# Kernel tuning notes

Hardware: AMD Instinct MI355X
Metric: run time of the kernel (lower is better)

The kernel has to match this reference:

```python
import jax, jax.numpy as jnp
import numpy as np

B, N, D = 4, 2048, 256
H = 8
HD = D // H
FF = 1024
EPS = 1e-5


def layer_norm(x, g, b):
    mu = jnp.mean(x, axis=-1, keepdims=True)
    var = jnp.mean((x - mu) ** 2, axis=-1, keepdims=True)
    return (x - mu) * jax.lax.rsqrt(var + EPS) * g + b


def setup_inputs() -> dict:
    key = jax.random.key(0)
    ks = jax.random.split(key, 12)
    s = 0.02
    return {
        "tokens": jax.random.normal(ks[0], (B, N, D), dtype=jnp.float32),
        "key_padding_mask": jnp.zeros((B, N), dtype=bool),
        "ln1_g": jnp.ones((D,), jnp.float32),
        "ln1_b": jnp.zeros((D,), jnp.float32),
        "wq": jax.random.normal(ks[1], (D, D), jnp.float32) * s,
        "bq": jnp.zeros((D,), jnp.float32),
        "wk": jax.random.normal(ks[2], (D, D), jnp.float32) * s,
        "bk": jnp.zeros((D,), jnp.float32),
        "wv": jax.random.normal(ks[3], (D, D), jnp.float32) * s,
        "bv": jnp.zeros((D,), jnp.float32),
        "wo": jax.random.normal(ks[4], (D, D), jnp.float32) * s,
        "bo": jnp.zeros((D,), jnp.float32),
        "ln2_g": jnp.ones((D,), jnp.float32),
        "ln2_b": jnp.zeros((D,), jnp.float32),
        "w1": jax.random.normal(ks[5], (D, FF), jnp.float32) * s,
        "b1": jnp.zeros((FF,), jnp.float32),
        "w2": jax.random.normal(ks[6], (FF, D), jnp.float32) * s,
        "b2": jnp.zeros((D,), jnp.float32),
    }


def reference(tokens, key_padding_mask, ln1_g, ln1_b, wq, bq, wk, bk, wv, bv,
              wo, bo, ln2_g, ln2_b, w1, b1, w2, b2):
    x = tokens
    # --- self-attention sublayer (pre-LN) ---
    xn = layer_norm(x, ln1_g, ln1_b)
    q = (xn @ wq + bq).reshape(B, N, H, HD).transpose(0, 2, 1, 3)  # [B,H,N,HD]
    k = (xn @ wk + bk).reshape(B, N, H, HD).transpose(0, 2, 1, 3)
    v = (xn @ wv + bv).reshape(B, N, H, HD).transpose(0, 2, 1, 3)
    scores = jnp.einsum('bhqd,bhkd->bhqk', q, k) / np.sqrt(HD).astype(np.float32)
    scores = jnp.where(key_padding_mask[:, None, None, :], -jnp.inf, scores)
    probs = jax.nn.softmax(scores, axis=-1)
    attn = jnp.einsum('bhqk,bhkd->bhqd', probs, v)
    attn = attn.transpose(0, 2, 1, 3).reshape(B, N, D)
    x = x + (attn @ wo + bo)
    # --- feed-forward sublayer (pre-LN) ---
    xn2 = layer_norm(x, ln2_g, ln2_b)
    h = jax.nn.gelu(xn2 @ w1 + b1, approximate=False)  # torch GELU is exact erf
    x = x + (h @ w2 + b2)
    return x
```

## Files before the change

### kernel.cpp

```cpp
#include <hip/hip_runtime.h>
#include <cmath>

typedef __attribute__((ext_vector_type(8))) __bf16 bf16x8;
typedef __attribute__((ext_vector_type(4))) __bf16 bf16x4;
typedef __attribute__((ext_vector_type(4))) float  f32x4;

constexpr int NB   = 4;
constexpr int SEQ  = 2048;
constexpr int DM   = 256;
constexpr int NH   = 8;
constexpr int DH   = 32;
constexpr int DFF  = 1024;
constexpr int MTOK = NB * SEQ;

__global__ __launch_bounds__(256) void ln_kernel(const float* __restrict__ x,
                                                 const float* __restrict__ g,
                                                 const float* __restrict__ b,
                                                 __bf16* __restrict__ out) {
  int wave = threadIdx.x >> 6, lane = threadIdx.x & 63;
  int row = blockIdx.x * 4 + wave;
  const float* xr = x + (size_t)row * DM;
  f32x4 v = *(const f32x4*)(xr + lane * 4);
  float s  = v[0] + v[1] + v[2] + v[3];
  float sq = v[0]*v[0] + v[1]*v[1] + v[2]*v[2] + v[3]*v[3];
  #pragma unroll
  for (int off = 1; off < 64; off <<= 1) {
    s  += __shfl_xor(s, off);
    sq += __shfl_xor(sq, off);
  }
  float mu  = s * (1.0f / DM);
  float var = sq * (1.0f / DM) - mu * mu;
  float rs  = rsqrtf(var + 1e-5f);
  f32x4 gv = *(const f32x4*)(g + lane * 4);
  f32x4 bv = *(const f32x4*)(b + lane * 4);
  bf16x4 o;
  #pragma unroll
  for (int i = 0; i < 4; ++i) o[i] = (__bf16)((v[i] - mu) * rs * gv[i] + bv[i]);
  *(bf16x4*)(out + (size_t)row * DM + lane * 4) = o;
}

__global__ __launch_bounds__(256) void prep_kernel(
    const float* __restrict__ wq, const float* __restrict__ wk, const float* __restrict__ wv,
    const float* __restrict__ wo, const float* __restrict__ w1, const float* __restrict__ w2,
    const unsigned char* __restrict__ mask, const float* __restrict__ tokens,
    const float* __restrict__ ln1g, const float* __restrict__ ln1b,
    __bf16* __restrict__ wqkvT, __bf16* __restrict__ woT,
    __bf16* __restrict__ w1T, __bf16* __restrict__ w2T,
    float* __restrict__ madd_g, __bf16* __restrict__ xn1) {
  __shared__ float tile[32][33];
  int z = blockIdx.z;
  int tid = threadIdx.x;
  if (z == 6) {
    if (blockIdx.x) return;
    int idx = blockIdx.y * 256 + tid;
    madd_g[idx] = mask[idx] ? -__builtin_inff() : 0.0f;
    return;
  }
  if (z >= 7) {
    int lb = blockIdx.y * 32 + blockIdx.x;
    int row = (z - 7) * 4096 + lb * 4 + (tid >> 6);
    int lane = tid & 63;
    const float* xr = tokens + (size_t)row * DM;
    f32x4 v = *(const f32x4*)(xr + lane * 4);
    float s  = v[0] + v[1] + v[2] + v[3];
    float sq = v[0]*v[0] + v[1]*v[1] + v[2]*v[2] + v[3]*v[3];
    #pragma unroll
    for (int off = 1; off < 64; off <<= 1) {
      s  += __shfl_xor(s, off);
      sq += __shfl_xor(sq, off);
    }
    float mu  = s * (1.0f / DM);
    float var = sq * (1.0f / DM) - mu * mu;
    float rs  = rsqrtf(var + 1e-5f);
    f32x4 gv = *(const f32x4*)(ln1g + lane * 4);
    f32x4 bv = *(const f32x4*)(ln1b + lane * 4);
    bf16x4 o;
    #pragma unroll
    for (int i = 0; i < 4; ++i) o[i] = (__bf16)((v[i] - mu) * rs * gv[i] + bv[i]);
    *(bf16x4*)(xn1 + (size_t)row * DM + lane * 4) = o;
    return;
  }
  const float* W; __bf16* Wt; int K, N;
  if      (z == 0) { W = wq; Wt = wqkvT;          K = 256;  N = 256;  }
  else if (z == 1) { W = wk; Wt = wqkvT + 65536;  K = 256;  N = 256;  }
  else if (z == 2) { W = wv; Wt = wqkvT + 131072; K = 256;  N = 256;  }
  else if (z == 3) { W = wo; Wt = woT;            K = 256;  N = 256;  }
  else if (z == 4) { W = w1; Wt = w1T;            K = 256;  N = 1024; }
  else             { W = w2; Wt = w2T;            K = 1024; N = 256;  }
  int n0 = blockIdx.x * 32, k0 = blockIdx.y * 32;
  if (n0 >= N || k0 >= K) return;
  {
    int kl = tid >> 3, n4 = (tid & 7) * 4;
    f32x4 v = *(const f32x4*)(W + (size_t)(k0 + kl) * N + n0 + n4);
    tile[kl][n4 + 0] = v[0]; tile[kl][n4 + 1] = v[1];
    tile[kl][n4 + 2] = v[2]; tile[kl][n4 + 3] = v[3];
  }
  __syncthreads();
  {
    int nl = tid >> 3, k4 = (tid & 7) * 4;
    bf16x4 o;
    #pragma unroll
    for (int i = 0; i < 4; ++i) o[i] = (__bf16)tile[k4 + i][nl];
    *(bf16x4*)(Wt + (size_t)(n0 + nl) * K + k0 + k4) = o;
  }
}

__global__ __launch_bounds__(256) void transpose_v(const __bf16* __restrict__ V,
                                                   __bf16* __restrict__ Vt) {
  __shared__ __bf16 tile[64][40];
  int tok0 = blockIdx.x * 64;
  int bh = blockIdx.y;
  int tid = threadIdx.x;
  {
    int tl = tid >> 2, h8 = (tid & 3) * 8;
    *(bf16x8*)&tile[tl][h8] = *(const bf16x8*)(V + ((size_t)bh * SEQ + tok0 + tl) * DH + h8);
  }
  __syncthreads();
  {
    int hl = tid >> 3, t8 = (tid & 7) * 8;
    bf16x8 o;
    #pragma unroll
    for (int i = 0; i < 8; ++i) o[i] = tile[t8 + i][hl];
    *(bf16x8*)(Vt + ((size_t)bh * DH + hl) * SEQ + tok0 + t8) = o;
  }
}

template<int BM, int BN, int EP>
__global__ __launch_bounds__(256) void gemm_bt(
    const __bf16* __restrict__ A, const __bf16* __restrict__ Bt,
    int M, int N, int K,
    const float* __restrict__ bias,
    const float* __restrict__ bq, const float* __restrict__ bk, const float* __restrict__ bv,
    const float* __restrict__ resid, float* __restrict__ outf,
    __bf16* __restrict__ outb,
    __bf16* __restrict__ outq, __bf16* __restrict__ outk, __bf16* __restrict__ outv) {
  constexpr int MT = BM / 32, NT = BN / 32;
  __shared__ __bf16 As[BM][72];
  __shared__ __bf16 Bs[BN][72];
  int tid = threadIdx.x;
  int wave = tid >> 6, lane = tid & 63;
  int wm = wave >> 1, wn = wave & 1;
  int quad = lane >> 4, l16 = lane & 15;
  int m0 = blockIdx.x * BM, n0 = blockIdx.y * BN;

  f32x4 acc[MT][NT];
  #pragma unroll
  for (int mt = 0; mt < MT; ++mt)
    #pragma unroll
    for (int nt = 0; nt < NT; ++nt)
      #pragma unroll
      for (int r = 0; r < 4; ++r) acc[mt][nt][r] = 0.0f;

  for (int kt = 0; kt < K; kt += 64) {
    __syncthreads();
    #pragma unroll
    for (int p = 0; p < BM / 32; ++p) {
      int idx = p * 256 + tid, row = idx >> 3, c8 = (idx & 7) * 8;
      *(bf16x8*)&As[row][c8] = *(const bf16x8*)(A + (size_t)(m0 + row) * K + kt + c8);
    }
    #pragma unroll
    for (int p = 0; p < BN / 32; ++p) {
      int idx = p * 256 + tid, row = idx >> 3, c8 = (idx & 7) * 8;
      *(bf16x8*)&Bs[row][c8] = *(const bf16x8*)(Bt + (size_t)(n0 + row) * K + kt + c8);
    }
    __syncthreads();
    #pragma unroll
    for (int ks = 0; ks < 2; ++ks) {
      bf16x8 af[MT], bfr[NT];
      #pragma unroll
      for (int mt = 0; mt < MT; ++mt)
        af[mt] = *(const bf16x8*)&As[wm * (BM / 2) + mt * 16 + l16][ks * 32 + quad * 8];
      #pragma unroll
      for (int nt = 0; nt < NT; ++nt)
        bfr[nt] = *(const bf16x8*)&Bs[wn * (BN / 2) + nt * 16 + l16][ks * 32 + quad * 8];
      #pragma unroll
      for (int mt = 0; mt < MT; ++mt)
        #pragma unroll
        for (int nt = 0; nt < NT; ++nt)
          acc[mt][nt] = __builtin_amdgcn_mfma_f32_16x16x32_bf16(af[mt], bfr[nt], acc[mt][nt], 0, 0, 0);
    }
  }

  #pragma unroll
  for (int mt = 0; mt < MT; ++mt)
  #pragma unroll
  for (int nt = 0; nt < NT; ++nt)
  #pragma unroll
  for (int r = 0; r < 4; ++r) {
    int gm = m0 + wm * (BM / 2) + mt * 16 + quad * 4 + r;
    int gn = n0 + wn * (BN / 2) + nt * 16 + l16;
    float v = acc[mt][nt][r];
    if constexpr (EP == 0) {
      int which = gn >> 8, nn = gn & 255;
      const float* bp = which == 0 ? bq : (which == 1 ? bk : bv);
      v += bp[nn];
      int h = nn >> 5, hd = nn & 31;
      int bb = gm >> 11, tok = gm & 2047;
      __bf16* dst = which == 0 ? outq : (which == 1 ? outk : outv);
      dst[(((size_t)(bb * NH + h)) * SEQ + tok) * DH + hd] = (__bf16)v;
    } else if constexpr (EP == 1) {
      v += bias[gn] + resid[(size_t)gm * N + gn];
      outf[(size_t)gm * N + gn] = v;
    } else {
      v += bias[gn];
      outb[(size_t)gm * N + gn] = (__bf16)(0.5f * v * (1.0f + erff(v * 0.70710678118654752f)));
    }
  }
}

__global__ __launch_bounds__(256) void attn_kernel(
    const __bf16* __restrict__ Q, const __bf16* __restrict__ K,
    const __bf16* __restrict__ Vt, const float* __restrict__ madd_g,
    __bf16* __restrict__ out) {
  constexpr float C2 = 0.2550350030061664f;
  __shared__ __bf16 Ks[64][40];
  __shared__ __bf16 Vs[48][72];
  __shared__ __bf16 Ps[4][16][72];
  int bh = blockIdx.x;
  int q0 = blockIdx.y * 64;
  int b  = bh >> 3, h = bh & 7;
  int tid = threadIdx.x;
  int wave = tid >> 6, lane = tid & 63;
  int quad = lane >> 4, l16 = lane & 15;
  const __bf16* Qb = Q  + (size_t)bh * SEQ * DH;
  const __bf16* Kb = K  + (size_t)bh * SEQ * DH;
  const __bf16* Vb = Vt + (size_t)bh * DH * SEQ;
  const float* maddb = madd_g + b * SEQ;
  int qw = q0 + wave * 16;

  if (tid < 32) ((unsigned int*)&Vs[32][0])[tid] = 0x3F803F80u;

  bf16x8 qf = *(const bf16x8*)(Qb + (size_t)(qw + l16) * DH + quad * 8);

  f32x4 o[2], ol;
  #pragma unroll
  for (int nt = 0; nt < 2; ++nt)
    #pragma unroll
    for (int r = 0; r < 4; ++r) o[nt][r] = 0.0f;
  #pragma unroll
  for (int r = 0; r < 4; ++r) ol[r] = 0.0f;

  for (int kt = 0; kt < SEQ / 64; ++kt) {
    int k0 = kt * 64;
    __syncthreads();
    { int row = tid >> 2, c8 = (tid & 3) * 8;
      *(bf16x8*)&Ks[row][c8] = *(const bf16x8*)(Kb + (size_t)(k0 + row) * DH + c8); }
    { int row = tid >> 3, c8 = (tid & 7) * 8;
      *(bf16x8*)&Vs[row][c8] = *(const bf16x8*)(Vb + (size_t)row * SEQ + k0 + c8); }
    __syncthreads();

    f32x4 md[4];
    #pragma unroll
    for (int mt = 0; mt < 4; ++mt)
      md[mt] = *(const f32x4*)(maddb + k0 + mt * 16 + quad * 4);

    f32x4 s[4];
    f32x4 zf; zf[0] = zf[1] = zf[2] = zf[3] = 0.0f;
    #pragma unroll
    for (int mt = 0; mt < 4; ++mt) {
      bf16x8 kf = *(const bf16x8*)&Ks[mt * 16 + l16][quad * 8];
      s[mt] = __builtin_amdgcn_mfma_f32_16x16x32_bf16(kf, qf, zf, 0, 0, 0);
    }

    #pragma unroll
    for (int mt = 0; mt < 4; ++mt) {
      bf16x4 pv;
      #pragma unroll
      for (int r = 0; r < 4; ++r)
        pv[r] = (__bf16)exp2f(fmaf(s[mt][r], C2, md[mt][r]));
      *(bf16x4*)&Ps[wave][l16][mt * 16 + quad * 4] = pv;
    }

    #pragma unroll
    for (int ks = 0; ks < 2; ++ks) {
      bf16x8 pf = *(const bf16x8*)&Ps[wave][l16][ks * 32 + quad * 8];
      #pragma unroll
      for (int nt = 0; nt < 2; ++nt) {
        bf16x8 vf = *(const bf16x8*)&Vs[nt * 16 + l16][ks * 32 + quad * 8];
        o[nt] = __builtin_amdgcn_mfma_f32_16x16x32_bf16(pf, vf, o[nt], 0, 0, 0);
      }
      bf16x8 vf1 = *(const bf16x8*)&Vs[32 + l16][ks * 32 + quad * 8];
      ol = __builtin_amdgcn_mfma_f32_16x16x32_bf16(pf, vf1, ol, 0, 0, 0);
    }
  }

  float inv[4];
  #pragma unroll
  for (int r = 0; r < 4; ++r) inv[r] = 1.0f / __shfl(ol[r], quad * 16);
  #pragma unroll
  for (int nt = 0; nt < 2; ++nt)
  #pragma unroll
  for (int r = 0; r < 4; ++r) {
    int q   = qw + quad * 4 + r;
    int col = h * DH + nt * 16 + l16;
    out[((size_t)(b * SEQ + q)) * DM + col] = (__bf16)(o[nt][r] * inv[r]);
  }
}

extern "C" void kernel_launch(void* const* d_in, const int* in_sizes, int n_in,
                              void* d_out, int out_size, void* d_ws, size_t ws_size,
                              hipStream_t stream) {
  const float* tokens = (const float*)d_in[0];
  const unsigned char* mask = (const unsigned char*)d_in[1];
  const float* ln1g = (const float*)d_in[2];
  const float* ln1b = (const float*)d_in[3];
  const float* wq = (const float*)d_in[4];
  const float* bq = (const float*)d_in[5];
  const float* wk = (const float*)d_in[6];
  const float* bk = (const float*)d_in[7];
  const float* wv = (const float*)d_in[8];
  const float* bv = (const float*)d_in[9];
  const float* wo = (const float*)d_in[10];
  const float* bo = (const float*)d_in[11];
  const float* ln2g = (const float*)d_in[12];
  const float* ln2b = (const float*)d_in[13];
  const float* w1 = (const float*)d_in[14];
  const float* b1 = (const float*)d_in[15];
  const float* w2 = (const float*)d_in[16];
  const float* b2 = (const float*)d_in[17];
  float* out = (float*)d_out;
  char* ws = (char*)d_ws;

  __bf16* wqkvT = (__bf16*)(ws + 0);
  __bf16* woT   = (__bf16*)(ws + 393216);
  __bf16* w1T   = (__bf16*)(ws + 524288);
  __bf16* w2T   = (__bf16*)(ws + 1048576);
  __bf16* xn1   = (__bf16*)(ws + 1572864);
  __bf16* qb    = (__bf16*)(ws + 5767168);
  __bf16* kb    = (__bf16*)(ws + 9961472);
  __bf16* vb    = (__bf16*)(ws + 14155776);
  __bf16* vt    = (__bf16*)(ws + 18350080);
  __bf16* attn  = (__bf16*)(ws + 22544384);
  float*  x1    = (float*)(ws + 26738688);
  __bf16* xn2   = (__bf16*)(ws + 35127296);
  __bf16* hbuf  = (__bf16*)(ws + 39321600);
  float*  madd  = (float*)(ws + 56098816);

  prep_kernel<<<dim3(32, 32, 9), 256, 0, stream>>>(
      wq, wk, wv, wo, w1, w2, mask, tokens, ln1g, ln1b,
      wqkvT, woT, w1T, w2T, madd, xn1);

  gemm_bt<64, 64, 0><<<dim3(128, 12), 256, 0, stream>>>(
      xn1, wqkvT, MTOK, 768, 256, nullptr, bq, bk, bv,
      nullptr, nullptr, nullptr, qb, kb, vb);

  transpose_v<<<dim3(SEQ / 64, 32), 256, 0, stream>>>(vb, vt);

  attn_kernel<<<dim3(32, SEQ / 64), 256, 0, stream>>>(qb, kb, vt, madd, attn);

  gemm_bt<64, 64, 1><<<dim3(128, 4), 256, 0, stream>>>(
      attn, woT, MTOK, 256, 256, bo, nullptr, nullptr, nullptr,
      tokens, x1, nullptr, nullptr, nullptr, nullptr);

  ln_kernel<<<MTOK / 4, 256, 0, stream>>>(x1, ln2g, ln2b, xn2);

  gemm_bt<64, 64, 2><<<dim3(128, 16), 256, 0, stream>>>(
      xn2, w1T, MTOK, DFF, 256, b1, nullptr, nullptr, nullptr,
      nullptr, nullptr, hbuf, nullptr, nullptr, nullptr);

  gemm_bt<64, 64, 1><<<dim3(128, 4), 256, 0, stream>>>(
      hbuf, w2T, MTOK, 256, DFF, b2, nullptr, nullptr, nullptr,
      x1, out, nullptr, nullptr, nullptr, nullptr);
}
```

Baseline: 215.3 us.

## Enlarge attention key tile, use register ones for rowsum, retile GEMMs

The attention kernel now processes 128 keys per iteration instead of 64, which halves the number of block barriers and tile loads. The row-sum MFMA takes a register vector of ones instead of an extra row of ones in shared memory, which also removes the final shuffle. exp2f becomes the hardware builtin, and the mask load moves into the exp loop. All GEMM launches switch to larger 128-row (and 128-column) tiles, giving fewer blocks, higher reuse and more LDS per block, at the risk of lower occupancy and poorer wave balance across CUs.

```diff
diff --git a/kernel.cpp b/kernel.cpp
--- a/kernel.cpp
+++ b/kernel.cpp
@@ -213,9 +213,9 @@
     const __bf16* __restrict__ Vt, const float* __restrict__ madd_g,
     __bf16* __restrict__ out) {
   constexpr float C2 = 0.2550350030061664f;
-  __shared__ __bf16 Ks[64][40];
-  __shared__ __bf16 Vs[48][72];
-  __shared__ __bf16 Ps[4][16][72];
+  __shared__ __bf16 Ks[128][40];
+  __shared__ __bf16 Vs[32][136];
+  __shared__ __bf16 Ps[4][16][136];
   int bh = blockIdx.x;
   int q0 = blockIdx.y * 64;
   int b  = bh >> 3, h = bh & 7;
@@ -228,10 +228,12 @@
   const float* maddb = madd_g + b * SEQ;
   int qw = q0 + wave * 16;
 
-  if (tid < 32) ((unsigned int*)&Vs[32][0])[tid] = 0x3F803F80u;
-
   bf16x8 qf = *(const bf16x8*)(Qb + (size_t)(qw + l16) * DH + quad * 8);
 
+  bf16x8 ones;
+  #pragma unroll
+  for (int i = 0; i < 8; ++i) ones[i] = (__bf16)1.0f;
+
   f32x4 o[2], ol;
   #pragma unroll
   for (int nt = 0; nt < 2; ++nt)
@@ -240,60 +242,60 @@
   #pragma unroll
   for (int r = 0; r < 4; ++r) ol[r] = 0.0f;
 
-  for (int kt = 0; kt < SEQ / 64; ++kt) {
-    int k0 = kt * 64;
+  for (int kt = 0; kt < SEQ / 128; ++kt) {
+    int k0 = kt * 128;
     __syncthreads();
-    { int row = tid >> 2, c8 = (tid & 3) * 8;
-      *(bf16x8*)&Ks[row][c8] = *(const bf16x8*)(Kb + (size_t)(k0 + row) * DH + c8); }
-    { int row = tid >> 3, c8 = (tid & 7) * 8;
-      *(bf16x8*)&Vs[row][c8] = *(const bf16x8*)(Vb + (size_t)row * SEQ + k0 + c8); }
+    #pragma unroll
+    for (int p = 0; p < 2; ++p) {
+      int idx = p * 256 + tid, row = idx >> 2, c8 = (idx & 3) * 8;
+      *(bf16x8*)&Ks[row][c8] = *(const bf16x8*)(Kb + (size_t)(k0 + row) * DH + c8);
+    }
+    #pragma unroll
+    for (int p = 0; p < 2; ++p) {
+      int idx = p * 256 + tid, row = idx >> 4, c8 = (idx & 15) * 8;
+      *(bf16x8*)&Vs[row][c8] = *(const bf16x8*)(Vb + (size_t)row * SEQ + k0 + c8);
+    }
     __syncthreads();
 
-    f32x4 md[4];
-    #pragma unroll
-    for (int mt = 0; mt < 4; ++mt)
-      md[mt] = *(const f32x4*)(maddb + k0 + mt * 16 + quad * 4);
-
-    f32x4 s[4];
+    f32x4 s[8];
     f32x4 zf; zf[0] = zf[1] = zf[2] = zf[3] = 0.0f;
     #pragma unroll
-    for (int mt = 0; mt < 4; ++mt) {
+    for (int mt = 0; mt < 8; ++mt) {
       bf16x8 kf = *(const bf16x8*)&Ks[mt * 16 + l16][quad * 8];
       s[mt] = __builtin_amdgcn_mfma_f32_16x16x32_bf16(kf, qf, zf, 0, 0, 0);
     }
 
     #pragma unroll
-    for (int mt = 0; mt < 4; ++mt) {
+    for (int mt = 0; mt < 8; ++mt) {
+      f32x4 md = *(const f32x4*)(maddb + k0 + mt * 16 + quad * 4);
       bf16x4 pv;
       #pragma unroll
       for (int r = 0; r < 4; ++r)
-        pv[r] = (__bf16)exp2f(fmaf(s[mt][r], C2, md[mt][r]));
+        pv[r] = (__bf16)__builtin_amdgcn_exp2f(fmaf(s[mt][r], C2, md[r]));
       *(bf16x4*)&Ps[wave][l16][mt * 16 + quad * 4] = pv;
     }
 
     #pragma unroll
-    for (int ks = 0; ks < 2; ++ks) {
+    for (int ks = 0; ks < 4; ++ks) {
       bf16x8 pf = *(const bf16x8*)&Ps[wave][l16][ks * 32 + quad * 8];
       #pragma unroll
       for (int nt = 0; nt < 2; ++nt) {
         bf16x8 vf = *(const bf16x8*)&Vs[nt * 16 + l16][ks * 32 + quad * 8];
         o[nt] = __builtin_amdgcn_mfma_f32_16x16x32_bf16(pf, vf, o[nt], 0, 0, 0);
       }
-      bf16x8 vf1 = *(const bf16x8*)&Vs[32 + l16][ks * 32 + quad * 8];
-      ol = __builtin_amdgcn_mfma_f32_16x16x32_bf16(pf, vf1, ol, 0, 0, 0);
-    }
-  }
-
-  float inv[4];
-  #pragma unroll
-  for (int r = 0; r < 4; ++r) inv[r] = 1.0f / __shfl(ol[r], quad * 16);
+      ol = __builtin_amdgcn_mfma_f32_16x16x32_bf16(pf, ones, ol, 0, 0, 0);
+    }
+  }
+
+  #pragma unroll
+  for (int r = 0; r < 4; ++r) ol[r] = 1.0f / ol[r];
   #pragma unroll
   for (int nt = 0; nt < 2; ++nt)
   #pragma unroll
   for (int r = 0; r < 4; ++r) {
     int q   = qw + quad * 4 + r;
     int col = h * DH + nt * 16 + l16;
-    out[((size_t)(b * SEQ + q)) * DM + col] = (__bf16)(o[nt][r] * inv[r]);
+    out[((size_t)(b * SEQ + q)) * DM + col] = (__bf16)(o[nt][r] * ol[r]);
   }
 }
 
@@ -340,7 +342,7 @@
       wq, wk, wv, wo, w1, w2, mask, tokens, ln1g, ln1b,
       wqkvT, woT, w1T, w2T, madd, xn1);
 
-  gemm_bt<64, 64, 0><<<dim3(128, 12), 256, 0, stream>>>(
+  gemm_bt<128, 128, 0><<<dim3(64, 6), 256, 0, stream>>>(
       xn1, wqkvT, MTOK, 768, 256, nullptr, bq, bk, bv,
       nullptr, nullptr, nullptr, qb, kb, vb);
 
@@ -348,17 +350,17 @@
 
   attn_kernel<<<dim3(32, SEQ / 64), 256, 0, stream>>>(qb, kb, vt, madd, attn);
 
-  gemm_bt<64, 64, 1><<<dim3(128, 4), 256, 0, stream>>>(
+  gemm_bt<128, 64, 1><<<dim3(64, 4), 256, 0, stream>>>(
       attn, woT, MTOK, 256, 256, bo, nullptr, nullptr, nullptr,
       tokens, x1, nullptr, nullptr, nullptr, nullptr);
 
   ln_kernel<<<MTOK / 4, 256, 0, stream>>>(x1, ln2g, ln2b, xn2);
 
-  gemm_bt<64, 64, 2><<<dim3(128, 16), 256, 0, stream>>>(
+  gemm_bt<128, 128, 2><<<dim3(64, 8), 256, 0, stream>>>(
       xn2, w1T, MTOK, DFF, 256, b1, nullptr, nullptr, nullptr,
       nullptr, nullptr, hbuf, nullptr, nullptr, nullptr);
 
-  gemm_bt<64, 64, 1><<<dim3(128, 4), 256, 0, stream>>>(
+  gemm_bt<128, 64, 1><<<dim3(64, 4), 256, 0, stream>>>(
       hbuf, w2T, MTOK, 256, DFF, b2, nullptr, nullptr, nullptr,
       x1, out, nullptr, nullptr, nullptr, nullptr);
 }
```

Result: no change. 214.6 us (-0.3%).
